# Kernel optimization log

Measured on AMD Instinct MI355X. Metric: run time of the kernel, lower is better.

The kernel has to match this reference:

```python
import jax, jax.numpy as jnp
import numpy as np

B, S, D, L = 64, 512, 768, 2


def setup_inputs() -> dict:
    key = jax.random.key(0)
    ks = jax.random.split(key, 8)
    sc = 1.0 / np.sqrt(D)
    sequence_output = jax.random.normal(ks[0], (B, S, D), dtype=jnp.float32)
    sot_positions = jax.random.randint(ks[1], (B, S), 0, 2, dtype=jnp.int32)
    # guarantee every sample has at least one selected token (torch nonzero-gather assumes this)
    sot_positions = sot_positions.at[:, 0].set(1)
    W_ih = jax.random.uniform(ks[2], (3 * D, D), jnp.float32, -sc, sc)
    W_hh = jax.random.uniform(ks[3], (3 * D, D), jnp.float32, -sc, sc)
    b_ih = jax.random.uniform(ks[4], (3 * D,), jnp.float32, -sc, sc)
    b_hh = jax.random.uniform(ks[5], (3 * D,), jnp.float32, -sc, sc)
    W_cls = jax.random.uniform(ks[6], (L, D), jnp.float32, -sc, sc)
    b_cls = jax.random.uniform(ks[7], (L,), jnp.float32, -sc, sc)
    return {"sequence_output": sequence_output, "sot_positions": sot_positions,
            "W_ih": W_ih, "W_hh": W_hh, "b_ih": b_ih, "b_hh": b_hh,
            "W_cls": W_cls, "b_cls": b_cls}


def _masked_gru_last(seq, mask, W_ih, W_hh, b_ih, b_hh):
    """Equivalent to: per sample, gather tokens where mask!=0, run a 1-layer GRU
    over that subsequence, return the final hidden state. Vectorized as a scan
    over time that freezes the hidden state at non-selected positions."""
    # precompute input projections for all timesteps: [B,S,3D]
    x_proj = jnp.einsum('bsd,ed->bse', seq, W_ih) + b_ih
    xs = (jnp.swapaxes(x_proj, 0, 1), jnp.swapaxes(mask, 0, 1))  # time-major
    h0 = jnp.zeros((seq.shape[0], W_hh.shape[1]), seq.dtype)

    def step(h, inp):
        xp, m = inp  # xp: [B,3D], m: [B]
        hp = h @ W_hh.T + b_hh  # [B,3D]
        xr, xz, xn = jnp.split(xp, 3, axis=-1)
        hr, hz, hn = jnp.split(hp, 3, axis=-1)
        r = jax.nn.sigmoid(xr + hr)
        z = jax.nn.sigmoid(xz + hz)
        n = jnp.tanh(xn + r * hn)
        h_new = (1.0 - z) * n + z * h
        h = jnp.where((m != 0)[:, None], h_new, h)
        return h, None

    h_last, _ = jax.lax.scan(step, h0, xs)
    return h_last  # [B,D]


def reference(sequence_output, sot_positions, W_ih, W_hh, b_ih, b_hh, W_cls, b_cls):
    match_vec = _masked_gru_last(sequence_output, sot_positions, W_ih, W_hh, b_ih, b_hh)
    # dropout is identity at eval time
    logits = match_vec @ W_cls.T + b_cls  # [B,L]
    return jax.nn.softmax(logits, axis=1)
```

## Files before the change

### kernel.cpp

```cpp
#include <hip/hip_runtime.h>
#include <hip/hip_bf16.h>


#define NB 64
#define NS 512
#define ND 768
#define TD 2304
#define NM 24

typedef __attribute__((ext_vector_type(4))) float f32x4;
typedef __attribute__((ext_vector_type(8))) short bf16x8;
typedef __attribute__((ext_vector_type(4))) unsigned int u32x4;

__device__ inline unsigned short f2bf(float f) {
  union { float f; unsigned u; } a; a.f = f;
  unsigned r = a.u + 0x7fff + ((a.u >> 16) & 1);
  return (unsigned short)(r >> 16);
}
__device__ inline float bf2f(unsigned short s) {
  union { unsigned u; float f; } a; a.u = ((unsigned)s) << 16;
  return a.f;
}

__device__ inline int load_flag(const int* p) {
  int v;
  asm volatile("global_load_dword %0, %1, off sc0 sc1\n\ts_waitcnt vmcnt(0)"
               : "=v"(v) : "v"(p) : "memory");
  return v;
}
__device__ inline void store_flag(int* p, int v) {
  asm volatile("global_store_dword %0, %1, off sc0 sc1"
               :: "v"(p), "v"(v) : "memory");
}
__device__ inline void store_h16(void* p, u32x4 v) {
  asm volatile("global_store_dwordx4 %0, %1, off sc0 sc1"
               :: "v"(p), "v"(v) : "memory");
}
__device__ inline void load2_h16(const void* p0, const void* p1,
                                 u32x4& a, u32x4& b) {
  asm volatile("global_load_dwordx4 %0, %2, off sc0 sc1\n\t"
               "global_load_dwordx4 %1, %3, off sc0 sc1\n\t"
               "s_waitcnt vmcnt(0)"
               : "=&v"(a), "=&v"(b) : "v"(p0), "v"(p1) : "memory");
}
__device__ inline void waitcnt_vm0() {
  asm volatile("s_waitcnt vmcnt(0)" ::: "memory");
}

__global__ void cvt_f32_bf16(const float* __restrict__ in,
                             unsigned short* __restrict__ out, int n) {
  int i = (blockIdx.x * blockDim.x + threadIdx.x) * 4;
  int stride = gridDim.x * blockDim.x * 4;
  for (; i < n; i += stride) {
    float4 v = *(const float4*)(in + i);
    ushort4 o;
    o.x = f2bf(v.x); o.y = f2bf(v.y); o.z = f2bf(v.z); o.w = f2bf(v.w);
    *(ushort4*)(out + i) = o;
  }
}

__global__ void compact_pos(const int* __restrict__ sot,
                            int* __restrict__ pos, int* __restrict__ ctrl) {
  int b = blockIdx.x, t = threadIdx.x;
  int m = (sot[b * NS + t] != 0) ? 1 : 0;
  unsigned long long ball = __ballot(m);
  int wid = t >> 6, lane = t & 63;
  __shared__ int wcnt[8];
  int prefix = __popcll(ball & ((1ull << lane) - 1ull));
  if (lane == 63) wcnt[wid] = __popcll(ball);
  __syncthreads();
  int base = 0;
  for (int w = 0; w < wid; ++w) base += wcnt[w];
  if (m) pos[b * NS + base + prefix] = t;
  if (t == 511) {
    int total = base + wcnt[7];
    ctrl[b] = total;
    atomicMax(&ctrl[64], total);
  }
}

#define BM 128
#define BN 256
__global__ __launch_bounds__(256) void gemm_xg(
    const float* __restrict__ seq,
    const int* __restrict__ pos,
    const int* __restrict__ ctrl,
    const unsigned short* __restrict__ Bg,
    const float* __restrict__ bias,
    unsigned short* __restrict__ C) {
  const int cntmax = ctrl[64];
  const int m0 = blockIdx.x * BM;
  if (m0 >= cntmax * 64) return;
  const int n0 = blockIdx.y * BN;
  __shared__ unsigned short lA[BM * 64];
  __shared__ unsigned short lB[BN * 64];
  const int tid = threadIdx.x;
  const int wid = tid >> 6, lane = tid & 63;
  const int wm = (wid & 1) * 64, wn = (wid >> 1) * 128;

  f32x4 acc[4][8];
#pragma unroll
  for (int i = 0; i < 4; ++i)
#pragma unroll
    for (int j = 0; j < 8; ++j) { f32x4 z = {0.f,0.f,0.f,0.f}; acc[i][j] = z; }

  for (int kt = 0; kt < 12; ++kt) {
    __syncthreads();
#pragma unroll
    for (int c = 0; c < 4; ++c) {
      int idx = c * 256 + tid;
      int r = idx >> 3, ch = idx & 7;
      int gm = m0 + r, ks = gm >> 6, ss = gm & 63;
      float4 v0 = {0,0,0,0}, v1 = {0,0,0,0};
      if (ks < ctrl[ss]) {
        int t = pos[ss * NS + ks];
        const float* src = seq + ((size_t)ss * NS + t) * ND + kt * 64 + ch * 8;
        v0 = *(const float4*)src;
        v1 = *(const float4*)(src + 4);
      }
      uint4 o;
      o.x = f2bf(v0.x) | ((unsigned)f2bf(v0.y) << 16);
      o.y = f2bf(v0.z) | ((unsigned)f2bf(v0.w) << 16);
      o.z = f2bf(v1.x) | ((unsigned)f2bf(v1.y) << 16);
      o.w = f2bf(v1.z) | ((unsigned)f2bf(v1.w) << 16);
      *(uint4*)((char*)lA + r * 128 + ((ch * 16) ^ ((r & 7) << 4))) = o;
    }
#pragma unroll
    for (int c = 0; c < 8; ++c) {
      int idx = c * 256 + tid;
      int r = idx >> 3, ch = idx & 7;
      uint4 v = *(const uint4*)(Bg + (size_t)(n0 + r) * ND + kt * 64 + ch * 8);
      *(uint4*)((char*)lB + r * 128 + ((ch * 16) ^ ((r & 7) << 4))) = v;
    }
    __syncthreads();
#pragma unroll
    for (int kk = 0; kk < 2; ++kk) {
      bf16x8 af[4], bfr[8];
      int kb = kk * 64 + (lane >> 4) * 16;
#pragma unroll
      for (int i = 0; i < 4; ++i) {
        int rowA = wm + i * 16 + (lane & 15);
        af[i] = *(const bf16x8*)((const char*)lA + rowA * 128 + (kb ^ ((rowA & 7) << 4)));
      }
#pragma unroll
      for (int i = 0; i < 8; ++i) {
        int rowB = wn + i * 16 + (lane & 15);
        bfr[i] = *(const bf16x8*)((const char*)lB + rowB * 128 + (kb ^ ((rowB & 7) << 4)));
      }
#pragma unroll
      for (int mi = 0; mi < 4; ++mi)
#pragma unroll
        for (int ni = 0; ni < 8; ++ni)
          acc[mi][ni] = __builtin_amdgcn_mfma_f32_16x16x32_bf16(
              af[mi], bfr[ni], acc[mi][ni], 0, 0, 0);
    }
  }
#pragma unroll
  for (int mi = 0; mi < 4; ++mi)
#pragma unroll
    for (int ni = 0; ni < 8; ++ni) {
      int col = n0 + wn + ni * 16 + (lane & 15);
      float bv = bias[col];
#pragma unroll
      for (int j = 0; j < 4; ++j) {
        int row = m0 + wm + mi * 16 + (lane >> 4) * 4 + j;
        C[(size_t)row * TD + col] = f2bf(acc[mi][ni][j] + bv);
      }
    }
}

__global__ __launch_bounds__(384) void rnn_gang(
    const unsigned short* __restrict__ xg,
    const unsigned short* __restrict__ whhb,
    const float* __restrict__ bhh,
    const int* __restrict__ ctrl,
    int* __restrict__ flags,
    unsigned short* __restrict__ Hb,
    const float* __restrict__ wcls,
    float* __restrict__ partial) {
  const int g  = blockIdx.x & 7;
  const int m  = blockIdx.x >> 3;
  const int d0 = m * 32;
  const int t  = threadIdx.x;
  const int w  = t >> 6;
  const int lane = t & 63;
  const int c  = lane & 15;
  const int kg = lane >> 4;

  __shared__ __align__(16) char Hl[8 * 1536];
  __shared__ __align__(16) float hp[8][100];
  __shared__ __align__(16) unsigned short hstage[256];

  const int lr = w * 16 + c;
  const int grow = (lr >> 5) * ND + d0 + (lr & 31);
  bf16x8 afr[24];
#pragma unroll
  for (int kt = 0; kt < 24; ++kt)
    afr[kt] = *(const bf16x8*)(whhb + (size_t)grow * ND + kt * 32 + kg * 8);

  const int s  = (t >> 5) & 7;
  const int d  = t & 31;
  const int sg = g * 8 + s;
  float br = 0.f, bz = 0.f, bn = 0.f, h = 0.f;
  int cnt_s = 0;
  if (t < 256) {
    br = bhh[d0 + d]; bz = bhh[ND + d0 + d]; bn = bhh[2 * ND + d0 + d];
    cnt_s = ctrl[sg];
  }
  int Kg = 0;
  for (int i = 0; i < 8; ++i) Kg = max(Kg, ctrl[g * 8 + i]);
  int* FG = flags + g * NM * 16;
  const int pm = lane < NM ? lane : (lane < 2 * NM ? lane - NM : lane - 2 * NM);

  if (t < 32) {
    u32x4 z = {0u, 0u, 0u, 0u};
    store_h16(Hb + ((size_t)(g * 8 + (t >> 2))) * ND + d0 + (t & 3) * 8, z);
    store_h16(Hb + ((size_t)(64 + g * 8 + (t >> 2))) * ND + d0 + (t & 3) * 8, z);
  }
  waitcnt_vm0();
  __syncthreads();
  if (t == 0) store_flag(&FG[m * 16], 1);

  int dead = 0;
  for (int k = 0; k < Kg; ++k) {
    float xr = 0.f, xz = 0.f, xn = 0.f;
    if (t < 256) {
      const unsigned short* xrow = xg + ((size_t)k * 64 + sg) * TD + d0 + d;
      xr = bf2f(xrow[0]); xz = bf2f(xrow[ND]); xn = bf2f(xrow[2 * ND]);
    }
    if (w == 0 && !dead) {
      const int* fp = &FG[pm * 16];
      int spins = 0;
      while (true) {
        int v = load_flag(fp);
        if (__all(v >= k + 1)) break;
        if (++spins > (1 << 20)) { dead = 1; break; }
      }
    }
    __syncthreads();
    {
      const unsigned short* hsrc = Hb + ((size_t)(k & 1) * 64 + g * 8) * ND;
      int i1 = t + 384;
      int r0 = t / 96, c0 = t - r0 * 96;
      int r1 = i1 / 96, c1 = i1 - r1 * 96;
      u32x4 a0, a1;
      load2_h16(hsrc + r0 * ND + c0 * 8, hsrc + r1 * ND + c1 * 8, a0, a1);
      *(u32x4*)(Hl + r0 * 1536 + ((c0 * 16) ^ ((r0 & 7) << 4))) = a0;
      *(u32x4*)(Hl + r1 * 1536 + ((c1 * 16) ^ ((r1 & 7) << 4))) = a1;
    }
    __syncthreads();
    f32x4 acc = {0.f, 0.f, 0.f, 0.f};
#pragma unroll
    for (int kt = 0; kt < 24; ++kt) {
      bf16x8 bfr = *(const bf16x8*)(Hl + (c & 7) * 1536 +
                    ((kt * 64 + kg * 16) ^ ((c & 7) << 4)));
      acc = __builtin_amdgcn_mfma_f32_16x16x32_bf16(afr[kt], bfr, acc, 0, 0, 0);
    }
    if (c < 8) *(f32x4*)&hp[c][w * 16 + kg * 4] = acc;
    __syncthreads();
    if (t < 256) {
      float ar = hp[s][d]      + br;
      float az = hp[s][32 + d] + bz;
      float an = hp[s][64 + d] + bn;
      float r  = 1.f / (1.f + __expf(-(xr + ar)));
      float z  = 1.f / (1.f + __expf(-(xz + az)));
      float nn = tanhf(xn + r * an);
      float hn = (1.f - z) * nn + z * h;
      if (k < cnt_s) h = hn;
      hstage[(s << 5) | d] = f2bf(h);
    }
    __syncthreads();
    if (t < 32) {
      u32x4 q = *(const u32x4*)((const char*)hstage + (t >> 2) * 64 + (t & 3) * 16);
      store_h16(Hb + ((size_t)((k + 1) & 1) * 64 + g * 8 + (t >> 2)) * ND + d0 + (t & 3) * 8, q);
    }
    waitcnt_vm0();
    if (t == 0) store_flag(&FG[m * 16], k + 2);
  }

  if (t < 256) {
    float p0 = h * wcls[d0 + d];
    float p1 = h * wcls[ND + d0 + d];
#pragma unroll
    for (int off = 16; off; off >>= 1) {
      p0 += __shfl_xor(p0, off);
      p1 += __shfl_xor(p1, off);
    }
    if (d == 0) {
      partial[(size_t)(m * 64 + sg) * 2]     = p0;
      partial[(size_t)(m * 64 + sg) * 2 + 1] = p1;
    }
  }
}

__global__ void finalize(const float* __restrict__ partial,
                         const float* __restrict__ bcls,
                         float* __restrict__ out) {
  int s = threadIdx.x;
  float l0 = bcls[0], l1 = bcls[1];
  for (int m = 0; m < NM; ++m) {
    l0 += partial[(size_t)(m * 64 + s) * 2];
    l1 += partial[(size_t)(m * 64 + s) * 2 + 1];
  }
  float mx = fmaxf(l0, l1);
  float e0 = __expf(l0 - mx), e1 = __expf(l1 - mx);
  float inv = 1.f / (e0 + e1);
  out[2 * s]     = e0 * inv;
  out[2 * s + 1] = e1 * inv;
}

extern "C" void kernel_launch(void* const* d_in, const int* in_sizes, int n_in,
                              void* d_out, int out_size, void* d_ws, size_t ws_size,
                              hipStream_t stream) {
  const float* seq  = (const float*)d_in[0];
  const int*   sot  = (const int*)d_in[1];
  const float* Wih  = (const float*)d_in[2];
  const float* Whh  = (const float*)d_in[3];
  const float* bih  = (const float*)d_in[4];
  const float* bhh  = (const float*)d_in[5];
  const float* Wcls = (const float*)d_in[6];
  const float* bcls = (const float*)d_in[7];
  float* out = (float*)d_out;

  char* ws = (char*)d_ws;
  unsigned short* xg   = (unsigned short*)(ws);
  unsigned short* wihb = (unsigned short*)(ws + 150994944);
  unsigned short* whhb = (unsigned short*)(ws + 154533888);
  int*            pos  = (int*)(ws + 158072832);
  int*            ctrl = (int*)(ws + 158203904);
  int*            flg  = (int*)(ws + 158204416);
  unsigned short* Hb   = (unsigned short*)(ws + 158216704);
  float*          part = (float*)(ws + 158413312);

  cvt_f32_bf16<<<1728, 256, 0, stream>>>(Wih, wihb, TD * ND);
  cvt_f32_bf16<<<1728, 256, 0, stream>>>(Whh, whhb, TD * ND);
  hipMemsetAsync(ctrl, 0, 512 + 12288, stream);
  compact_pos<<<NB, NS, 0, stream>>>(sot, pos, ctrl);
  gemm_xg<<<dim3(NB * NS / BM, TD / BN), 256, 0, stream>>>(seq, pos, ctrl, wihb, bih, xg);
  rnn_gang<<<192, 384, 0, stream>>>(xg, whhb, bhh, ctrl, flg, Hb, Wcls, part);
  finalize<<<1, 64, 0, stream>>>(part, bcls, out);
}
```

Baseline: 962.3 us.

## Replace per-block flag polling with per-thread canary flags and prefetch inputs

```diff
diff --git a/kernel.cpp b/kernel.cpp
--- a/kernel.cpp
+++ b/kernel.cpp
@@ -22,11 +22,11 @@
   return a.f;
 }
 
-__device__ inline int load_flag(const int* p) {
-  int v;
-  asm volatile("global_load_dword %0, %1, off sc0 sc1\n\ts_waitcnt vmcnt(0)"
-               : "=v"(v) : "v"(p) : "memory");
-  return v;
+__device__ inline void load2_flag(const int* p0, const int* p1, int& a, int& b) {
+  asm volatile("global_load_dword %0, %2, off sc0 sc1\n\t"
+               "global_load_dword %1, %3, off sc0 sc1\n\t"
+               "s_waitcnt vmcnt(0)"
+               : "=&v"(a), "=&v"(b) : "v"(p0), "v"(p1) : "memory");
 }
 __device__ inline void store_flag(int* p, int v) {
   asm volatile("global_store_dword %0, %1, off sc0 sc1"
@@ -174,7 +174,7 @@
     const unsigned short* __restrict__ whhb,
     const float* __restrict__ bhh,
     const int* __restrict__ ctrl,
-    int* __restrict__ flags,
+    int* __restrict__ canary,
     unsigned short* __restrict__ Hb,
     const float* __restrict__ wcls,
     float* __restrict__ partial) {
@@ -209,44 +209,50 @@
   }
   int Kg = 0;
   for (int i = 0; i < 8; ++i) Kg = max(Kg, ctrl[g * 8 + i]);
-  int* FG = flags + g * NM * 16;
-  const int pm = lane < NM ? lane : (lane < 2 * NM ? lane - NM : lane - 2 * NM);
+  unsigned short* HG = Hb + (size_t)g * 8 * ND;
+  int* CG = canary + g * 256;
+
+  const int i0 = t, i1 = t + 384;
+  const int r0 = i0 / 96, c0 = i0 - r0 * 96;
+  const int r1 = i1 / 96, c1 = i1 - r1 * 96;
+  const int* cy0 = CG + (c0 >> 2) * 8 + r0;
+  const int* cy1 = CG + (c1 >> 2) * 8 + r1;
 
   if (t < 32) {
     u32x4 z = {0u, 0u, 0u, 0u};
-    store_h16(Hb + ((size_t)(g * 8 + (t >> 2))) * ND + d0 + (t & 3) * 8, z);
-    store_h16(Hb + ((size_t)(64 + g * 8 + (t >> 2))) * ND + d0 + (t & 3) * 8, z);
+    store_h16(HG + (t >> 2) * ND + d0 + (t & 3) * 8, z);
   }
   waitcnt_vm0();
-  __syncthreads();
-  if (t == 0) store_flag(&FG[m * 16], 1);
+  if (t < 8) store_flag(&CG[m * 8 + t], 1);
+
+  float xr = 0.f, xz = 0.f, xn = 0.f;
+  if (t < 256) {
+    const unsigned short* xrow = xg + (size_t)sg * TD + d0 + d;
+    xr = bf2f(xrow[0]); xz = bf2f(xrow[ND]); xn = bf2f(xrow[2 * ND]);
+  }
 
   int dead = 0;
   for (int k = 0; k < Kg; ++k) {
-    float xr = 0.f, xz = 0.f, xn = 0.f;
-    if (t < 256) {
-      const unsigned short* xrow = xg + ((size_t)k * 64 + sg) * TD + d0 + d;
-      xr = bf2f(xrow[0]); xz = bf2f(xrow[ND]); xn = bf2f(xrow[2 * ND]);
-    }
-    if (w == 0 && !dead) {
-      const int* fp = &FG[pm * 16];
-      int spins = 0;
-      while (true) {
-        int v = load_flag(fp);
-        if (__all(v >= k + 1)) break;
-        if (++spins > (1 << 20)) { dead = 1; break; }
-      }
-    }
-    __syncthreads();
     {
-      const unsigned short* hsrc = Hb + ((size_t)(k & 1) * 64 + g * 8) * ND;
-      int i1 = t + 384;
-      int r0 = t / 96, c0 = t - r0 * 96;
-      int r1 = i1 / 96, c1 = i1 - r1 * 96;
+      const unsigned tk = (unsigned)(k + 1);
+      if (!dead) {
+        int spins = 0, v0, v1;
+        for (;;) {
+          load2_flag(cy0, cy1, v0, v1);
+          if ((unsigned)v0 >= tk && (unsigned)v1 >= tk) break;
+          if (++spins > (1 << 20)) { dead = 1; break; }
+        }
+      }
       u32x4 a0, a1;
-      load2_h16(hsrc + r0 * ND + c0 * 8, hsrc + r1 * ND + c1 * 8, a0, a1);
+      load2_h16(HG + r0 * ND + c0 * 8, HG + r1 * ND + c1 * 8, a0, a1);
       *(u32x4*)(Hl + r0 * 1536 + ((c0 * 16) ^ ((r0 & 7) << 4))) = a0;
       *(u32x4*)(Hl + r1 * 1536 + ((c1 * 16) ^ ((r1 & 7) << 4))) = a1;
+    }
+    float nxr = 0.f, nxz = 0.f, nxn = 0.f;
+    if (t < 256) {
+      int kn = (k + 1 < Kg) ? k + 1 : k;
+      const unsigned short* xrow = xg + ((size_t)kn * 64 + sg) * TD + d0 + d;
+      nxr = bf2f(xrow[0]); nxz = bf2f(xrow[ND]); nxn = bf2f(xrow[2 * ND]);
     }
     __syncthreads();
     f32x4 acc = {0.f, 0.f, 0.f, 0.f};
@@ -269,13 +275,14 @@
       if (k < cnt_s) h = hn;
       hstage[(s << 5) | d] = f2bf(h);
     }
+    xr = nxr; xz = nxz; xn = nxn;
     __syncthreads();
     if (t < 32) {
       u32x4 q = *(const u32x4*)((const char*)hstage + (t >> 2) * 64 + (t & 3) * 16);
-      store_h16(Hb + ((size_t)((k + 1) & 1) * 64 + g * 8 + (t >> 2)) * ND + d0 + (t & 3) * 8, q);
+      store_h16(HG + (t >> 2) * ND + d0 + (t & 3) * 8, q);
     }
     waitcnt_vm0();
-    if (t == 0) store_flag(&FG[m * 16], k + 2);
+    if (t < 8) store_flag(&CG[m * 8 + t], k + 2);
   }
 
   if (t < 256) {
@@ -328,15 +335,15 @@
   unsigned short* whhb = (unsigned short*)(ws + 154533888);
   int*            pos  = (int*)(ws + 158072832);
   int*            ctrl = (int*)(ws + 158203904);
-  int*            flg  = (int*)(ws + 158204416);
-  unsigned short* Hb   = (unsigned short*)(ws + 158216704);
-  float*          part = (float*)(ws + 158413312);
+  int*            cn   = (int*)(ws + 158204416);
+  unsigned short* Hb   = (unsigned short*)(ws + 158212608);
+  float*          part = (float*)(ws + 158310912);
 
   cvt_f32_bf16<<<1728, 256, 0, stream>>>(Wih, wihb, TD * ND);
   cvt_f32_bf16<<<1728, 256, 0, stream>>>(Whh, whhb, TD * ND);
-  hipMemsetAsync(ctrl, 0, 512 + 12288, stream);
+  hipMemsetAsync(ctrl, 0, 512 + 8192, stream);
   compact_pos<<<NB, NS, 0, stream>>>(sot, pos, ctrl);
   gemm_xg<<<dim3(NB * NS / BM, TD / BN), 256, 0, stream>>>(seq, pos, ctrl, wihb, bih, xg);
-  rnn_gang<<<192, 384, 0, stream>>>(xg, whhb, bhh, ctrl, flg, Hb, Wcls, part);
+  rnn_gang<<<192, 384, 0, stream>>>(xg, whhb, bhh, ctrl, cn, Hb, Wcls, part);
   finalize<<<1, 64, 0, stream>>>(part, bcls, out);
 }
```

After: 1.142 ms. 18.7% more time.

## Fuse input-projection GEMM into persistent GRU kernel with per-chunk readiness flags

Applied to the files above, without the earlier changes.

```diff
diff --git a/kernel.cpp b/kernel.cpp
--- a/kernel.cpp
+++ b/kernel.cpp
@@ -7,6 +7,10 @@
 #define ND 768
 #define TD 2304
 #define NM 24
+#define HXE 49152
+#define NT 12
+#define NWORK 256
+#define RNNB 192
 
 typedef __attribute__((ext_vector_type(4))) float f32x4;
 typedef __attribute__((ext_vector_type(8))) short bf16x8;
@@ -42,6 +46,21 @@
                "global_load_dwordx4 %1, %3, off sc0 sc1\n\t"
                "s_waitcnt vmcnt(0)"
                : "=&v"(a), "=&v"(b) : "v"(p0), "v"(p1) : "memory");
+}
+__device__ inline void load3_u16(const unsigned short* p0,
+                                 const unsigned short* p1,
+                                 const unsigned short* p2,
+                                 unsigned& a, unsigned& b, unsigned& c) {
+  asm volatile("global_load_ushort %0, %3, off sc0 sc1\n\t"
+               "global_load_ushort %1, %4, off sc0 sc1\n\t"
+               "global_load_ushort %2, %5, off sc0 sc1\n\t"
+               "s_waitcnt vmcnt(0)"
+               : "=&v"(a), "=&v"(b), "=&v"(c)
+               : "v"(p0), "v"(p1), "v"(p2) : "memory");
+}
+__device__ inline void store_u16_sc(unsigned short* p, unsigned v) {
+  asm volatile("global_store_short %0, %1, off sc0 sc1"
+               :: "v"(p), "v"(v) : "memory");
 }
 __device__ inline void waitcnt_vm0() {
   asm volatile("s_waitcnt vmcnt(0)" ::: "memory");
@@ -79,117 +98,115 @@
   }
 }
 
-#define BM 128
-#define BN 256
-__global__ __launch_bounds__(256) void gemm_xg(
+__global__ __launch_bounds__(384) void rnn_fused(
     const float* __restrict__ seq,
     const int* __restrict__ pos,
     const int* __restrict__ ctrl,
-    const unsigned short* __restrict__ Bg,
-    const float* __restrict__ bias,
-    unsigned short* __restrict__ C) {
-  const int cntmax = ctrl[64];
-  const int m0 = blockIdx.x * BM;
-  if (m0 >= cntmax * 64) return;
-  const int n0 = blockIdx.y * BN;
-  __shared__ unsigned short lA[BM * 64];
-  __shared__ unsigned short lB[BN * 64];
-  const int tid = threadIdx.x;
-  const int wid = tid >> 6, lane = tid & 63;
-  const int wm = (wid & 1) * 64, wn = (wid >> 1) * 128;
-
-  f32x4 acc[4][8];
-#pragma unroll
-  for (int i = 0; i < 4; ++i)
-#pragma unroll
-    for (int j = 0; j < 8; ++j) { f32x4 z = {0.f,0.f,0.f,0.f}; acc[i][j] = z; }
-
-  for (int kt = 0; kt < 12; ++kt) {
-    __syncthreads();
-#pragma unroll
-    for (int c = 0; c < 4; ++c) {
-      int idx = c * 256 + tid;
-      int r = idx >> 3, ch = idx & 7;
-      int gm = m0 + r, ks = gm >> 6, ss = gm & 63;
-      float4 v0 = {0,0,0,0}, v1 = {0,0,0,0};
-      if (ks < ctrl[ss]) {
-        int t = pos[ss * NS + ks];
-        const float* src = seq + ((size_t)ss * NS + t) * ND + kt * 64 + ch * 8;
-        v0 = *(const float4*)src;
-        v1 = *(const float4*)(src + 4);
-      }
-      uint4 o;
-      o.x = f2bf(v0.x) | ((unsigned)f2bf(v0.y) << 16);
-      o.y = f2bf(v0.z) | ((unsigned)f2bf(v0.w) << 16);
-      o.z = f2bf(v1.x) | ((unsigned)f2bf(v1.y) << 16);
-      o.w = f2bf(v1.z) | ((unsigned)f2bf(v1.w) << 16);
-      *(uint4*)((char*)lA + r * 128 + ((ch * 16) ^ ((r & 7) << 4))) = o;
-    }
-#pragma unroll
-    for (int c = 0; c < 8; ++c) {
-      int idx = c * 256 + tid;
-      int r = idx >> 3, ch = idx & 7;
-      uint4 v = *(const uint4*)(Bg + (size_t)(n0 + r) * ND + kt * 64 + ch * 8);
-      *(uint4*)((char*)lB + r * 128 + ((ch * 16) ^ ((r & 7) << 4))) = v;
-    }
-    __syncthreads();
-#pragma unroll
-    for (int kk = 0; kk < 2; ++kk) {
-      bf16x8 af[4], bfr[8];
-      int kb = kk * 64 + (lane >> 4) * 16;
-#pragma unroll
-      for (int i = 0; i < 4; ++i) {
-        int rowA = wm + i * 16 + (lane & 15);
-        af[i] = *(const bf16x8*)((const char*)lA + rowA * 128 + (kb ^ ((rowA & 7) << 4)));
-      }
-#pragma unroll
-      for (int i = 0; i < 8; ++i) {
-        int rowB = wn + i * 16 + (lane & 15);
-        bfr[i] = *(const bf16x8*)((const char*)lB + rowB * 128 + (kb ^ ((rowB & 7) << 4)));
-      }
-#pragma unroll
-      for (int mi = 0; mi < 4; ++mi)
-#pragma unroll
-        for (int ni = 0; ni < 8; ++ni)
-          acc[mi][ni] = __builtin_amdgcn_mfma_f32_16x16x32_bf16(
-              af[mi], bfr[ni], acc[mi][ni], 0, 0, 0);
-    }
-  }
-#pragma unroll
-  for (int mi = 0; mi < 4; ++mi)
-#pragma unroll
-    for (int ni = 0; ni < 8; ++ni) {
-      int col = n0 + wn + ni * 16 + (lane & 15);
-      float bv = bias[col];
-#pragma unroll
-      for (int j = 0; j < 4; ++j) {
-        int row = m0 + wm + mi * 16 + (lane >> 4) * 4 + j;
-        C[(size_t)row * TD + col] = f2bf(acc[mi][ni][j] + bv);
-      }
-    }
-}
-
-__global__ __launch_bounds__(384) void rnn_gang(
-    const unsigned short* __restrict__ xg,
+    const unsigned short* __restrict__ wihb,
+    const float* __restrict__ bih,
+    unsigned short* __restrict__ xg,
+    int* __restrict__ xgdone,
     const unsigned short* __restrict__ whhb,
     const float* __restrict__ bhh,
-    const int* __restrict__ ctrl,
     int* __restrict__ flags,
     unsigned short* __restrict__ Hb,
     const float* __restrict__ wcls,
     float* __restrict__ partial) {
-  const int g  = blockIdx.x & 7;
-  const int m  = blockIdx.x >> 3;
+  __shared__ __align__(16) char LDSU[41472];
+  const int bid = blockIdx.x;
+  const int t = threadIdx.x;
+  const int w = t >> 6, lane = t & 63;
+
+  if (bid >= RNNB) {
+    const int cntmax = ctrl[64];
+    const int rowsNeeded = cntmax * 64;
+    const int wr = w & 1, wc = w >> 1;
+    unsigned short* lA = (unsigned short*)LDSU;
+    unsigned short* lB = (unsigned short*)(LDSU + 16384);
+
+    for (int T = bid - RNNB; T < 256 * NT; T += NWORK) {
+      const int kchunk = T / NT, ntile = T - kchunk * NT;
+      const int m0 = kchunk << 7;
+      if (m0 >= rowsNeeded) continue;
+      const int n0 = ntile * 192;
+      f32x4 acc[4][4];
+#pragma unroll
+      for (int i = 0; i < 4; ++i)
+#pragma unroll
+        for (int j = 0; j < 4; ++j) { f32x4 z = {0.f,0.f,0.f,0.f}; acc[i][j] = z; }
+
+      for (int kt = 0; kt < 12; ++kt) {
+        __syncthreads();
+        for (int idx = t; idx < 1024; idx += 384) {
+          int r = idx >> 3, ch = idx & 7;
+          int gm = m0 + r, ks = gm >> 6, ss = gm & 63;
+          float4 v0 = {0,0,0,0}, v1 = {0,0,0,0};
+          if (ks < ctrl[ss]) {
+            int tp = pos[ss * NS + ks];
+            const float* src = seq + ((size_t)ss * NS + tp) * ND + kt * 64 + ch * 8;
+            v0 = *(const float4*)src;
+            v1 = *(const float4*)(src + 4);
+          }
+          uint4 o;
+          o.x = f2bf(v0.x) | ((unsigned)f2bf(v0.y) << 16);
+          o.y = f2bf(v0.z) | ((unsigned)f2bf(v0.w) << 16);
+          o.z = f2bf(v1.x) | ((unsigned)f2bf(v1.y) << 16);
+          o.w = f2bf(v1.z) | ((unsigned)f2bf(v1.w) << 16);
+          *(uint4*)((char*)lA + r * 128 + ((ch * 16) ^ ((r & 7) << 4))) = o;
+        }
+        for (int idx = t; idx < 1536; idx += 384) {
+          int r = idx >> 3, ch = idx & 7;
+          uint4 v = *(const uint4*)(wihb + (size_t)(n0 + r) * ND + kt * 64 + ch * 8);
+          *(uint4*)((char*)lB + r * 128 + ((ch * 16) ^ ((r & 7) << 4))) = v;
+        }
+        __syncthreads();
+#pragma unroll
+        for (int kk = 0; kk < 2; ++kk) {
+          const int kb = kk * 64 + (lane >> 4) * 16;
+          bf16x8 af[4], bfr[4];
+#pragma unroll
+          for (int i = 0; i < 4; ++i) {
+            int rowA = wr * 64 + i * 16 + (lane & 15);
+            af[i] = *(const bf16x8*)((const char*)lA + rowA * 128 + (kb ^ ((rowA & 7) << 4)));
+            int rowB = wc * 64 + i * 16 + (lane & 15);
+            bfr[i] = *(const bf16x8*)((const char*)lB + rowB * 128 + (kb ^ ((rowB & 7) << 4)));
+          }
+#pragma unroll
+          for (int mi = 0; mi < 4; ++mi)
+#pragma unroll
+            for (int ni = 0; ni < 4; ++ni)
+              acc[mi][ni] = __builtin_amdgcn_mfma_f32_16x16x32_bf16(
+                  af[mi], bfr[ni], acc[mi][ni], 0, 0, 0);
+        }
+      }
+#pragma unroll
+      for (int mi = 0; mi < 4; ++mi)
+#pragma unroll
+        for (int ni = 0; ni < 4; ++ni) {
+          int col = n0 + wc * 64 + ni * 16 + (lane & 15);
+          float bv = bih[col];
+#pragma unroll
+          for (int j = 0; j < 4; ++j) {
+            int row = m0 + wr * 64 + mi * 16 + (lane >> 4) * 4 + j;
+            store_u16_sc(xg + (size_t)row * TD + col,
+                         (unsigned)f2bf(acc[mi][ni][j] + bv));
+          }
+        }
+      waitcnt_vm0();
+      __syncthreads();
+      if (t == 0) atomicAdd(&xgdone[kchunk], 1);
+    }
+    return;
+  }
+
+  const int g  = bid & 7;
+  const int m  = bid >> 3;
   const int d0 = m * 32;
-  const int t  = threadIdx.x;
-  const int w  = t >> 6;
-  const int lane = t & 63;
   const int c  = lane & 15;
   const int kg = lane >> 4;
 
-  __shared__ __align__(16) char Hl[8 * 1536];
-  __shared__ __align__(16) float hp[8][100];
-  __shared__ __align__(16) unsigned short hstage[256];
+  char* Hl = LDSU;
+  float (*hp)[100] = (float (*)[100])(void*)(LDSU + 12288);
 
   const int lr = w * 16 + c;
   const int grow = (lr >> 5) * ND + d0 + (lr & 31);
@@ -210,7 +227,6 @@
   int Kg = 0;
   for (int i = 0; i < 8; ++i) Kg = max(Kg, ctrl[g * 8 + i]);
   int* FG = flags + g * NM * 16;
-  const int pm = lane < NM ? lane : (lane < 2 * NM ? lane - NM : lane - 2 * NM);
 
   if (t < 32) {
     u32x4 z = {0u, 0u, 0u, 0u};
@@ -221,19 +237,37 @@
   __syncthreads();
   if (t == 0) store_flag(&FG[m * 16], 1);
 
+  if (w == 0) {
+    int spins = 0;
+    for (;;) {
+      int v = load_flag(&xgdone[0]);
+      if (__all(v >= NT)) break;
+      if (++spins > (1 << 20)) break;
+    }
+  }
+  __syncthreads();
+  float xr = 0.f, xz = 0.f, xn = 0.f;
+  if (t < 256) {
+    const unsigned short* xrow = xg + (size_t)sg * TD + d0 + d;
+    unsigned a, b2, c2;
+    load3_u16(xrow, xrow + ND, xrow + 2 * ND, a, b2, c2);
+    xr = bf2f((unsigned short)a); xz = bf2f((unsigned short)b2); xn = bf2f((unsigned short)c2);
+  }
+
   int dead = 0;
   for (int k = 0; k < Kg; ++k) {
-    float xr = 0.f, xz = 0.f, xn = 0.f;
-    if (t < 256) {
-      const unsigned short* xrow = xg + ((size_t)k * 64 + sg) * TD + d0 + d;
-      xr = bf2f(xrow[0]); xz = bf2f(xrow[ND]); xn = bf2f(xrow[2 * ND]);
-    }
+    const int kn = (k + 1 < Kg) ? (k + 1) : (Kg - 1);
     if (w == 0 && !dead) {
-      const int* fp = &FG[pm * 16];
+      const int* pp = (lane < NM) ? (const int*)&FG[lane * 16]
+                    : (lane == NM) ? (const int*)&xgdone[kn >> 1]
+                    : (const int*)&FG[0];
+      const unsigned tk = (unsigned)(k + 1);
       int spins = 0;
-      while (true) {
-        int v = load_flag(fp);
-        if (__all(v >= k + 1)) break;
+      for (;;) {
+        int v = load_flag(pp);
+        int ok = (lane < NM) ? ((unsigned)v >= tk)
+               : (lane == NM) ? (v >= NT) : 1;
+        if (__all(ok)) break;
         if (++spins > (1 << 20)) { dead = 1; break; }
       }
     }
@@ -247,6 +281,13 @@
       load2_h16(hsrc + r0 * ND + c0 * 8, hsrc + r1 * ND + c1 * 8, a0, a1);
       *(u32x4*)(Hl + r0 * 1536 + ((c0 * 16) ^ ((r0 & 7) << 4))) = a0;
       *(u32x4*)(Hl + r1 * 1536 + ((c1 * 16) ^ ((r1 & 7) << 4))) = a1;
+    }
+    float nxr = 0.f, nxz = 0.f, nxn = 0.f;
+    if (t < 256 && k + 1 < Kg) {
+      const unsigned short* xrow = xg + ((size_t)(k + 1) * 64 + sg) * TD + d0 + d;
+      unsigned a, b2, c2;
+      load3_u16(xrow, xrow + ND, xrow + 2 * ND, a, b2, c2);
+      nxr = bf2f((unsigned short)a); nxz = bf2f((unsigned short)b2); nxn = bf2f((unsigned short)c2);
     }
     __syncthreads();
     f32x4 acc = {0.f, 0.f, 0.f, 0.f};
@@ -267,14 +308,12 @@
       float nn = tanhf(xn + r * an);
       float hn = (1.f - z) * nn + z * h;
       if (k < cnt_s) h = hn;
-      hstage[(s << 5) | d] = f2bf(h);
-    }
+      store_u16_sc(Hb + (size_t)((k + 1) & 1) * HXE + (size_t)sg * ND + d0 + d,
+                   (unsigned)f2bf(h));
+    }
+    xr = nxr; xz = nxz; xn = nxn;
+    waitcnt_vm0();
     __syncthreads();
-    if (t < 32) {
-      u32x4 q = *(const u32x4*)((const char*)hstage + (t >> 2) * 64 + (t & 3) * 16);
-      store_h16(Hb + ((size_t)((k + 1) & 1) * 64 + g * 8 + (t >> 2)) * ND + d0 + (t & 3) * 8, q);
-    }
-    waitcnt_vm0();
     if (t == 0) store_flag(&FG[m * 16], k + 2);
   }
 
@@ -323,20 +362,21 @@
   float* out = (float*)d_out;
 
   char* ws = (char*)d_ws;
-  unsigned short* xg   = (unsigned short*)(ws);
-  unsigned short* wihb = (unsigned short*)(ws + 150994944);
-  unsigned short* whhb = (unsigned short*)(ws + 154533888);
-  int*            pos  = (int*)(ws + 158072832);
-  int*            ctrl = (int*)(ws + 158203904);
-  int*            flg  = (int*)(ws + 158204416);
-  unsigned short* Hb   = (unsigned short*)(ws + 158216704);
-  float*          part = (float*)(ws + 158413312);
+  unsigned short* xg     = (unsigned short*)(ws);
+  unsigned short* wihb   = (unsigned short*)(ws + 150994944);
+  unsigned short* whhb   = (unsigned short*)(ws + 154533888);
+  int*            pos    = (int*)(ws + 158072832);
+  int*            ctrl   = (int*)(ws + 158203904);
+  int*            flg    = (int*)(ws + 158204416);
+  int*            xgdone = (int*)(ws + 158216704);
+  unsigned short* Hb     = (unsigned short*)(ws + 158217728);
+  float*          part   = (float*)(ws + 158414336);
 
   cvt_f32_bf16<<<1728, 256, 0, stream>>>(Wih, wihb, TD * ND);
   cvt_f32_bf16<<<1728, 256, 0, stream>>>(Whh, whhb, TD * ND);
-  hipMemsetAsync(ctrl, 0, 512 + 12288, stream);
+  hipMemsetAsync(ctrl, 0, 512 + 12288 + 1024, stream);
   compact_pos<<<NB, NS, 0, stream>>>(sot, pos, ctrl);
-  gemm_xg<<<dim3(NB * NS / BM, TD / BN), 256, 0, stream>>>(seq, pos, ctrl, wihb, bih, xg);
-  rnn_gang<<<192, 384, 0, stream>>>(xg, whhb, bhh, ctrl, flg, Hb, Wcls, part);
+  rnn_fused<<<RNNB + NWORK, 384, 0, stream>>>(
+      seq, pos, ctrl, wihb, bih, xg, xgdone, whhb, bhh, flg, Hb, Wcls, part);
   finalize<<<1, 64, 0, stream>>>(part, bcls, out);
 }
```

Result: slower. 1.683 ms (+74.9%).

## Fuse input projection GEMM into persistent GRU kernel with prefetched x tiles

Applied to the files above, without the earlier changes.

```diff
diff --git a/kernel.cpp b/kernel.cpp
--- a/kernel.cpp
+++ b/kernel.cpp
@@ -5,8 +5,8 @@
 #define NB 64
 #define NS 512
 #define ND 768
-#define TD 2304
 #define NM 24
+#define HXE 49152
 
 typedef __attribute__((ext_vector_type(4))) float f32x4;
 typedef __attribute__((ext_vector_type(8))) short bf16x8;
@@ -17,9 +17,16 @@
   unsigned r = a.u + 0x7fff + ((a.u >> 16) & 1);
   return (unsigned short)(r >> 16);
 }
-__device__ inline float bf2f(unsigned short s) {
-  union { unsigned u; float f; } a; a.u = ((unsigned)s) << 16;
-  return a.f;
+__device__ inline unsigned pk2(float a, float b) {
+  return (unsigned)f2bf(a) | ((unsigned)f2bf(b) << 16);
+}
+__device__ inline bf16x8 pack8(float4 a, float4 b) {
+  bf16x8 r;
+  r[0] = (short)f2bf(a.x); r[1] = (short)f2bf(a.y);
+  r[2] = (short)f2bf(a.z); r[3] = (short)f2bf(a.w);
+  r[4] = (short)f2bf(b.x); r[5] = (short)f2bf(b.y);
+  r[6] = (short)f2bf(b.z); r[7] = (short)f2bf(b.w);
+  return r;
 }
 
 __device__ inline int load_flag(const int* p) {
@@ -45,18 +52,6 @@
 }
 __device__ inline void waitcnt_vm0() {
   asm volatile("s_waitcnt vmcnt(0)" ::: "memory");
-}
-
-__global__ void cvt_f32_bf16(const float* __restrict__ in,
-                             unsigned short* __restrict__ out, int n) {
-  int i = (blockIdx.x * blockDim.x + threadIdx.x) * 4;
-  int stride = gridDim.x * blockDim.x * 4;
-  for (; i < n; i += stride) {
-    float4 v = *(const float4*)(in + i);
-    ushort4 o;
-    o.x = f2bf(v.x); o.y = f2bf(v.y); o.z = f2bf(v.z); o.w = f2bf(v.w);
-    *(ushort4*)(out + i) = o;
-  }
 }
 
 __global__ void compact_pos(const int* __restrict__ sot,
@@ -79,101 +74,14 @@
   }
 }
 
-#define BM 128
-#define BN 256
-__global__ __launch_bounds__(256) void gemm_xg(
+__global__ __launch_bounds__(384) void rnn_gang(
     const float* __restrict__ seq,
     const int* __restrict__ pos,
     const int* __restrict__ ctrl,
-    const unsigned short* __restrict__ Bg,
-    const float* __restrict__ bias,
-    unsigned short* __restrict__ C) {
-  const int cntmax = ctrl[64];
-  const int m0 = blockIdx.x * BM;
-  if (m0 >= cntmax * 64) return;
-  const int n0 = blockIdx.y * BN;
-  __shared__ unsigned short lA[BM * 64];
-  __shared__ unsigned short lB[BN * 64];
-  const int tid = threadIdx.x;
-  const int wid = tid >> 6, lane = tid & 63;
-  const int wm = (wid & 1) * 64, wn = (wid >> 1) * 128;
-
-  f32x4 acc[4][8];
-#pragma unroll
-  for (int i = 0; i < 4; ++i)
-#pragma unroll
-    for (int j = 0; j < 8; ++j) { f32x4 z = {0.f,0.f,0.f,0.f}; acc[i][j] = z; }
-
-  for (int kt = 0; kt < 12; ++kt) {
-    __syncthreads();
-#pragma unroll
-    for (int c = 0; c < 4; ++c) {
-      int idx = c * 256 + tid;
-      int r = idx >> 3, ch = idx & 7;
-      int gm = m0 + r, ks = gm >> 6, ss = gm & 63;
-      float4 v0 = {0,0,0,0}, v1 = {0,0,0,0};
-      if (ks < ctrl[ss]) {
-        int t = pos[ss * NS + ks];
-        const float* src = seq + ((size_t)ss * NS + t) * ND + kt * 64 + ch * 8;
-        v0 = *(const float4*)src;
-        v1 = *(const float4*)(src + 4);
-      }
-      uint4 o;
-      o.x = f2bf(v0.x) | ((unsigned)f2bf(v0.y) << 16);
-      o.y = f2bf(v0.z) | ((unsigned)f2bf(v0.w) << 16);
-      o.z = f2bf(v1.x) | ((unsigned)f2bf(v1.y) << 16);
-      o.w = f2bf(v1.z) | ((unsigned)f2bf(v1.w) << 16);
-      *(uint4*)((char*)lA + r * 128 + ((ch * 16) ^ ((r & 7) << 4))) = o;
-    }
-#pragma unroll
-    for (int c = 0; c < 8; ++c) {
-      int idx = c * 256 + tid;
-      int r = idx >> 3, ch = idx & 7;
-      uint4 v = *(const uint4*)(Bg + (size_t)(n0 + r) * ND + kt * 64 + ch * 8);
-      *(uint4*)((char*)lB + r * 128 + ((ch * 16) ^ ((r & 7) << 4))) = v;
-    }
-    __syncthreads();
-#pragma unroll
-    for (int kk = 0; kk < 2; ++kk) {
-      bf16x8 af[4], bfr[8];
-      int kb = kk * 64 + (lane >> 4) * 16;
-#pragma unroll
-      for (int i = 0; i < 4; ++i) {
-        int rowA = wm + i * 16 + (lane & 15);
-        af[i] = *(const bf16x8*)((const char*)lA + rowA * 128 + (kb ^ ((rowA & 7) << 4)));
-      }
-#pragma unroll
-      for (int i = 0; i < 8; ++i) {
-        int rowB = wn + i * 16 + (lane & 15);
-        bfr[i] = *(const bf16x8*)((const char*)lB + rowB * 128 + (kb ^ ((rowB & 7) << 4)));
-      }
-#pragma unroll
-      for (int mi = 0; mi < 4; ++mi)
-#pragma unroll
-        for (int ni = 0; ni < 8; ++ni)
-          acc[mi][ni] = __builtin_amdgcn_mfma_f32_16x16x32_bf16(
-              af[mi], bfr[ni], acc[mi][ni], 0, 0, 0);
-    }
-  }
-#pragma unroll
-  for (int mi = 0; mi < 4; ++mi)
-#pragma unroll
-    for (int ni = 0; ni < 8; ++ni) {
-      int col = n0 + wn + ni * 16 + (lane & 15);
-      float bv = bias[col];
-#pragma unroll
-      for (int j = 0; j < 4; ++j) {
-        int row = m0 + wm + mi * 16 + (lane >> 4) * 4 + j;
-        C[(size_t)row * TD + col] = f2bf(acc[mi][ni][j] + bv);
-      }
-    }
-}
-
-__global__ __launch_bounds__(384) void rnn_gang(
-    const unsigned short* __restrict__ xg,
-    const unsigned short* __restrict__ whhb,
+    const float* __restrict__ whh,
+    const float* __restrict__ wih,
     const float* __restrict__ bhh,
-    const int* __restrict__ ctrl,
+    const float* __restrict__ bih,
     int* __restrict__ flags,
     unsigned short* __restrict__ Hb,
     const float* __restrict__ wcls,
@@ -188,23 +96,31 @@
   const int kg = lane >> 4;
 
   __shared__ __align__(16) char Hl[8 * 1536];
-  __shared__ __align__(16) float hp[8][100];
+  __shared__ __align__(16) char Xl[2 * 8 * 1536];
+  __shared__ __align__(16) float hp[8][136];
   __shared__ __align__(16) unsigned short hstage[256];
 
   const int lr = w * 16 + c;
   const int grow = (lr >> 5) * ND + d0 + (lr & 31);
-  bf16x8 afr[24];
-#pragma unroll
-  for (int kt = 0; kt < 24; ++kt)
-    afr[kt] = *(const bf16x8*)(whhb + (size_t)grow * ND + kt * 32 + kg * 8);
+  bf16x8 afr[24], air[24];
+#pragma unroll
+  for (int kt = 0; kt < 24; ++kt) {
+    const float* s1 = whh + (size_t)grow * ND + kt * 32 + kg * 8;
+    afr[kt] = pack8(*(const float4*)s1, *(const float4*)(s1 + 4));
+    const float* s2 = wih + (size_t)grow * ND + kt * 32 + kg * 8;
+    air[kt] = pack8(*(const float4*)s2, *(const float4*)(s2 + 4));
+  }
 
   const int s  = (t >> 5) & 7;
   const int d  = t & 31;
   const int sg = g * 8 + s;
-  float br = 0.f, bz = 0.f, bn = 0.f, h = 0.f;
+  float b_r = 0.f, b_z = 0.f, b_in = 0.f, b_hn = 0.f, h = 0.f;
   int cnt_s = 0;
   if (t < 256) {
-    br = bhh[d0 + d]; bz = bhh[ND + d0 + d]; bn = bhh[2 * ND + d0 + d];
+    b_r  = bih[d0 + d] + bhh[d0 + d];
+    b_z  = bih[ND + d0 + d] + bhh[ND + d0 + d];
+    b_in = bih[2 * ND + d0 + d];
+    b_hn = bhh[2 * ND + d0 + d];
     cnt_s = ctrl[sg];
   }
   int Kg = 0;
@@ -212,6 +128,13 @@
   int* FG = flags + g * NM * 16;
   const int pm = lane < NM ? lane : (lane < 2 * NM ? lane - NM : lane - 2 * NM);
 
+  const int xrow = t / 48;
+  const int xcol = (t - xrow * 48) * 16;
+  const int cnt_row = ctrl[g * 8 + xrow];
+  const float* xsrc_base = seq + (size_t)(g * 8 + xrow) * NS * ND + xcol;
+  const int* xpos_base = pos + (g * 8 + xrow) * NS;
+  const int xswz = (xrow & 7) << 4;
+
   if (t < 32) {
     u32x4 z = {0u, 0u, 0u, 0u};
     store_h16(Hb + ((size_t)(g * 8 + (t >> 2))) * ND + d0 + (t & 3) * 8, z);
@@ -221,23 +144,58 @@
   __syncthreads();
   if (t == 0) store_flag(&FG[m * 16], 1);
 
+  {
+    int p = xpos_base[0];
+    const float* src = xsrc_base + (size_t)p * ND;
+    float4 v0 = *(const float4*)src,      v1 = *(const float4*)(src + 4);
+    float4 v2 = *(const float4*)(src + 8), v3 = *(const float4*)(src + 12);
+    uint4 o0, o1;
+    o0.x = pk2(v0.x, v0.y); o0.y = pk2(v0.z, v0.w);
+    o0.z = pk2(v1.x, v1.y); o0.w = pk2(v1.z, v1.w);
+    o1.x = pk2(v2.x, v2.y); o1.y = pk2(v2.z, v2.w);
+    o1.z = pk2(v3.x, v3.y); o1.w = pk2(v3.z, v3.w);
+    char* xb = Xl + xrow * 1536;
+    *(uint4*)(xb + ((xcol * 2) ^ xswz)) = o0;
+    *(uint4*)(xb + ((xcol * 2 + 16) ^ xswz)) = o1;
+  }
+  __syncthreads();
+  f32x4 acc_x = {0.f, 0.f, 0.f, 0.f};
+#pragma unroll
+  for (int kt = 0; kt < 24; ++kt) {
+    bf16x8 bfr = *(const bf16x8*)(Xl + (c & 7) * 1536 +
+                  ((kt * 64 + kg * 16) ^ ((c & 7) << 4)));
+    acc_x = __builtin_amdgcn_mfma_f32_16x16x32_bf16(air[kt], bfr, acc_x, 0, 0, 0);
+  }
+
   int dead = 0;
   for (int k = 0; k < Kg; ++k) {
-    float xr = 0.f, xz = 0.f, xn = 0.f;
-    if (t < 256) {
-      const unsigned short* xrow = xg + ((size_t)k * 64 + sg) * TD + d0 + d;
-      xr = bf2f(xrow[0]); xz = bf2f(xrow[ND]); xn = bf2f(xrow[2 * ND]);
-    }
     if (w == 0 && !dead) {
       const int* fp = &FG[pm * 16];
+      const unsigned tk = (unsigned)(k + 1);
       int spins = 0;
       while (true) {
         int v = load_flag(fp);
-        if (__all(v >= k + 1)) break;
+        if (__all((unsigned)v >= tk)) break;
         if (++spins > (1 << 20)) { dead = 1; break; }
       }
     }
     __syncthreads();
+    {
+      int kk = (k + 1 < Kg) ? k + 1 : Kg - 1;
+      int idx = (kk < cnt_row) ? kk : cnt_row - 1;
+      int p = xpos_base[idx];
+      const float* src = xsrc_base + (size_t)p * ND;
+      float4 v0 = *(const float4*)src,      v1 = *(const float4*)(src + 4);
+      float4 v2 = *(const float4*)(src + 8), v3 = *(const float4*)(src + 12);
+      uint4 o0, o1;
+      o0.x = pk2(v0.x, v0.y); o0.y = pk2(v0.z, v0.w);
+      o0.z = pk2(v1.x, v1.y); o0.w = pk2(v1.z, v1.w);
+      o1.x = pk2(v2.x, v2.y); o1.y = pk2(v2.z, v2.w);
+      o1.z = pk2(v3.x, v3.y); o1.w = pk2(v3.z, v3.w);
+      char* xb = Xl + ((k + 1) & 1) * 12288 + xrow * 1536;
+      *(uint4*)(xb + ((xcol * 2) ^ xswz)) = o0;
+      *(uint4*)(xb + ((xcol * 2 + 16) ^ xswz)) = o1;
+    }
     {
       const unsigned short* hsrc = Hb + ((size_t)(k & 1) * 64 + g * 8) * ND;
       int i1 = t + 384;
@@ -249,22 +207,35 @@
       *(u32x4*)(Hl + r1 * 1536 + ((c1 * 16) ^ ((r1 & 7) << 4))) = a1;
     }
     __syncthreads();
-    f32x4 acc = {0.f, 0.f, 0.f, 0.f};
+    f32x4 acc;
+    if (w < 4) acc = acc_x;
+    else { f32x4 z = {0.f, 0.f, 0.f, 0.f}; acc = z; }
 #pragma unroll
     for (int kt = 0; kt < 24; ++kt) {
       bf16x8 bfr = *(const bf16x8*)(Hl + (c & 7) * 1536 +
                     ((kt * 64 + kg * 16) ^ ((c & 7) << 4)));
       acc = __builtin_amdgcn_mfma_f32_16x16x32_bf16(afr[kt], bfr, acc, 0, 0, 0);
     }
-    if (c < 8) *(f32x4*)&hp[c][w * 16 + kg * 4] = acc;
+    if (c < 8) {
+      *(f32x4*)&hp[c][w * 16 + kg * 4] = acc;
+      if (w >= 4)
+        *(f32x4*)&hp[c][96 + (w - 4) * 16 + kg * 4] = acc_x;
+    }
     __syncthreads();
+    {
+      const char* xb = Xl + ((k + 1) & 1) * 12288;
+      f32x4 z = {0.f, 0.f, 0.f, 0.f}; acc_x = z;
+#pragma unroll
+      for (int kt = 0; kt < 24; ++kt) {
+        bf16x8 bfr = *(const bf16x8*)(xb + (c & 7) * 1536 +
+                      ((kt * 64 + kg * 16) ^ ((c & 7) << 4)));
+        acc_x = __builtin_amdgcn_mfma_f32_16x16x32_bf16(air[kt], bfr, acc_x, 0, 0, 0);
+      }
+    }
     if (t < 256) {
-      float ar = hp[s][d]      + br;
-      float az = hp[s][32 + d] + bz;
-      float an = hp[s][64 + d] + bn;
-      float r  = 1.f / (1.f + __expf(-(xr + ar)));
-      float z  = 1.f / (1.f + __expf(-(xz + az)));
-      float nn = tanhf(xn + r * an);
+      float r  = 1.f / (1.f + __expf(-(hp[s][d] + b_r)));
+      float z  = 1.f / (1.f + __expf(-(hp[s][32 + d] + b_z)));
+      float nn = tanhf(hp[s][96 + d] + b_in + r * (hp[s][64 + d] + b_hn));
       float hn = (1.f - z) * nn + z * h;
       if (k < cnt_s) h = hn;
       hstage[(s << 5) | d] = f2bf(h);
@@ -272,7 +243,8 @@
     __syncthreads();
     if (t < 32) {
       u32x4 q = *(const u32x4*)((const char*)hstage + (t >> 2) * 64 + (t & 3) * 16);
-      store_h16(Hb + ((size_t)((k + 1) & 1) * 64 + g * 8 + (t >> 2)) * ND + d0 + (t & 3) * 8, q);
+      store_h16(Hb + (size_t)((k + 1) & 1) * HXE + (size_t)(g * 8 + (t >> 2)) * ND
+                + d0 + (t & 3) * 8, q);
     }
     waitcnt_vm0();
     if (t == 0) store_flag(&FG[m * 16], k + 2);
@@ -323,20 +295,15 @@
   float* out = (float*)d_out;
 
   char* ws = (char*)d_ws;
-  unsigned short* xg   = (unsigned short*)(ws);
-  unsigned short* wihb = (unsigned short*)(ws + 150994944);
-  unsigned short* whhb = (unsigned short*)(ws + 154533888);
-  int*            pos  = (int*)(ws + 158072832);
-  int*            ctrl = (int*)(ws + 158203904);
-  int*            flg  = (int*)(ws + 158204416);
-  unsigned short* Hb   = (unsigned short*)(ws + 158216704);
-  float*          part = (float*)(ws + 158413312);
-
-  cvt_f32_bf16<<<1728, 256, 0, stream>>>(Wih, wihb, TD * ND);
-  cvt_f32_bf16<<<1728, 256, 0, stream>>>(Whh, whhb, TD * ND);
+  int*            pos  = (int*)(ws);
+  int*            ctrl = (int*)(ws + 131072);
+  int*            flg  = (int*)(ws + 131584);
+  unsigned short* Hb   = (unsigned short*)(ws + 143872);
+  float*          part = (float*)(ws + 340480);
+
   hipMemsetAsync(ctrl, 0, 512 + 12288, stream);
   compact_pos<<<NB, NS, 0, stream>>>(sot, pos, ctrl);
-  gemm_xg<<<dim3(NB * NS / BM, TD / BN), 256, 0, stream>>>(seq, pos, ctrl, wihb, bih, xg);
-  rnn_gang<<<192, 384, 0, stream>>>(xg, whhb, bhh, ctrl, flg, Hb, Wcls, part);
+  rnn_gang<<<192, 384, 0, stream>>>(seq, pos, ctrl, Whh, Wih, bhh, bih,
+                                    flg, Hb, Wcls, part);
   finalize<<<1, 64, 0, stream>>>(part, bcls, out);
 }
```

Result: slower. 1.568 ms (+62.9%).
